# Kernel tuning notes

Measured on AMD Instinct MI355X. Metric: run time of the kernel, lower is better.

The kernel has to match this reference:

```python
import jax, jax.numpy as jnp
import numpy as np

B, T, D, H = 2, 2048, 1024, 16
Dh = D // H
MAX_LEN = 2048


def build_rope_cache(max_len, head_dim):
    theta = 10000.0 ** (-jnp.arange(0, head_dim, 2, dtype=jnp.float32) / head_dim)
    pos = jnp.arange(max_len, dtype=jnp.float32)
    angles = pos[:, None] * theta[None, :]          # [T, Dh/2]
    sin = jnp.sin(angles)[:, None, :]               # [T, 1, Dh/2]
    cos = jnp.cos(angles)[:, None, :]
    return sin, cos


def apply_rotary_pos_emb(q, k, sin, cos):
    q1, q2 = jnp.split(q, 2, axis=-1)
    k1, k2 = jnp.split(k, 2, axis=-1)
    q_out = jnp.concatenate([q1 * cos + q2 * sin, -q1 * sin + q2 * cos], axis=-1)
    k_out = jnp.concatenate([k1 * cos + k2 * sin, -k1 * sin + k2 * cos], axis=-1)
    return q_out, k_out


def setup_inputs() -> dict:
    key = jax.random.key(0)
    k1, k2, k3 = jax.random.split(key, 3)
    x = jax.random.normal(k1, (B, T, D), dtype=jnp.float32)
    W_qkv = jax.random.normal(k2, (D, 3 * D), dtype=jnp.float32) * (D ** -0.5)
    W_proj = jax.random.normal(k3, (D, D), dtype=jnp.float32) * (D ** -0.5)
    # causal mask: 1.0 where attention is disallowed (future positions)
    mask = jnp.triu(jnp.ones((T, T), dtype=jnp.float32), k=1)
    return {"x": x, "mask": mask, "W_qkv": W_qkv, "W_proj": W_proj}


def reference(x, mask, W_qkv, W_proj):
    b, t, d = x.shape
    qkv = x @ W_qkv                                  # [B,T,3D]
    q, k, v = jnp.split(qkv, 3, axis=-1)
    q = q.reshape(b, t, H, Dh)
    k = k.reshape(b, t, H, Dh)
    v = v.reshape(b, t, H, Dh)
    sin, cos = build_rope_cache(MAX_LEN, Dh)
    q, k = apply_rotary_pos_emb(q, k, sin[:t], cos[:t])
    scale = 1.0 / jnp.sqrt(jnp.float32(Dh))
    att = jnp.einsum('bthd,bThd->bhtT', q, k) * scale
    att = att + mask * -1e9                          # mask broadcasts [T,T]->[B,H,T,T]
    weights = jax.nn.softmax(att, axis=-1)
    out = jnp.einsum('bhtT,bThd->bthd', weights, v).reshape(b, t, d)
    return out @ W_proj
```

## Files before the change

### kernel.cpp

```cpp
#include <hip/hip_runtime.h>
#include <hip/hip_bf16.h>

typedef __bf16  bf16x8 __attribute__((ext_vector_type(8)));
typedef __bf16  bf16x4 __attribute__((ext_vector_type(4)));
typedef __bf16  bf16x2 __attribute__((ext_vector_type(2)));
typedef float   f32x4  __attribute__((ext_vector_type(4)));
typedef float   f32x16 __attribute__((ext_vector_type(16)));
typedef unsigned u32x4 __attribute__((ext_vector_type(4)));

#define MFMA16(a,b,c) __builtin_amdgcn_mfma_f32_16x16x32_bf16(a,b,c,0,0,0)
#define MFMA32(a,b,c) __builtin_amdgcn_mfma_f32_32x32x16_bf16(a,b,c,0,0,0)


struct bf4 { __hip_bfloat16 a,b,c,d; };

__global__ __launch_bounds__(256) void cast_f32_bf16(const float* __restrict__ in,
                                                     __hip_bfloat16* __restrict__ out,
                                                     int n4) {
  int i = blockIdx.x * 256 + threadIdx.x;
  if (i >= n4) return;
  float4 v = ((const float4*)in)[i];
  bf4 o { __float2bfloat16(v.x), __float2bfloat16(v.y),
          __float2bfloat16(v.z), __float2bfloat16(v.w) };
  ((bf4*)out)[i] = o;
}

__global__ __launch_bounds__(256) void transpose_cast(const float* __restrict__ W,
                                                      __hip_bfloat16* __restrict__ WT,
                                                      int R, int C) {
  __shared__ float tile[32][33];
  int c0 = blockIdx.x * 32, r0 = blockIdx.y * 32;
  int tx = threadIdx.x & 31, ty = threadIdx.x >> 5;
  #pragma unroll
  for (int i = 0; i < 32; i += 8)
    tile[ty + i][tx] = W[(size_t)(r0 + ty + i) * C + c0 + tx];
  __syncthreads();
  #pragma unroll
  for (int i = 0; i < 32; i += 8)
    WT[(size_t)(c0 + ty + i) * R + r0 + tx] = __float2bfloat16(tile[tx][ty + i]);
}

template <typename OutT>
__global__ __launch_bounds__(256) void gemm_bt(const __hip_bfloat16* __restrict__ A,
                                               const __hip_bfloat16* __restrict__ BT,
                                               OutT* __restrict__ C,
                                               int M, int N, int K) {
  __shared__ __hip_bfloat16 As[2][128][32];
  __shared__ __hip_bfloat16 Bs[2][128][32];
  int tid  = threadIdx.x;
  int lane = tid & 63, wid = tid >> 6;
  int wm = wid >> 1, wn = wid & 1;
  int rowBase = blockIdx.y * 128;
  int colBase = blockIdx.x * 128;
  int lr = lane & 15, lg = lane >> 4;

  f32x4 acc[4][4];
  #pragma unroll
  for (int i = 0; i < 4; ++i)
    #pragma unroll
    for (int j = 0; j < 4; ++j) acc[i][j] = f32x4{0.f,0.f,0.f,0.f};

  int nt = K >> 5;

#define GSTAGE(buf, kt)                                                                 \
  do {                                                                                  \
    int k0_ = (kt) << 5;                                                                \
    _Pragma("unroll")                                                                   \
    for (int p = 0; p < 2; ++p) {                                                       \
      int idx = p * 256 + tid;                                                          \
      int r_ = idx >> 2, sl_ = idx & 3;                                                 \
      __builtin_amdgcn_global_load_lds(                                                 \
        (const __attribute__((address_space(1))) unsigned int*)                         \
          &A[(size_t)(rowBase + r_) * K + k0_ + ((sl_ ^ (r_ & 3)) * 8)],                \
        (__attribute__((address_space(3))) unsigned int*)&As[buf][r_][sl_ * 8], 16, 0, 0);\
      __builtin_amdgcn_global_load_lds(                                                 \
        (const __attribute__((address_space(1))) unsigned int*)                         \
          &BT[(size_t)(colBase + r_) * K + k0_ + ((sl_ ^ (r_ & 3)) * 8)],               \
        (__attribute__((address_space(3))) unsigned int*)&Bs[buf][r_][sl_ * 8], 16, 0, 0);\
    }                                                                                   \
  } while (0)

  GSTAGE(0, 0);
  for (int t = 0; t < nt; ++t) {
    int cur = t & 1;
    if (t + 1 < nt) {
      GSTAGE(cur ^ 1, t + 1);
      asm volatile("s_waitcnt vmcnt(4)" ::: "memory");
    } else {
      asm volatile("s_waitcnt vmcnt(0)" ::: "memory");
    }
    __builtin_amdgcn_s_barrier();
    __builtin_amdgcn_sched_barrier(0);

    bf16x8 af[4], bfr[4];
    #pragma unroll
    for (int mf = 0; mf < 4; ++mf) {
      int row = wm*64 + mf*16 + lr;
      af[mf]  = *(const bf16x8*)&As[cur][row][((lg ^ (lr & 3)) * 8)];
    }
    #pragma unroll
    for (int nf = 0; nf < 4; ++nf) {
      int row = wn*64 + nf*16 + lr;
      bfr[nf] = *(const bf16x8*)&Bs[cur][row][((lg ^ (lr & 3)) * 8)];
    }
    #pragma unroll
    for (int mf = 0; mf < 4; ++mf)
      #pragma unroll
      for (int nf = 0; nf < 4; ++nf)
        acc[mf][nf] = MFMA16(af[mf], bfr[nf], acc[mf][nf]);

    __builtin_amdgcn_s_barrier();
  }
#undef GSTAGE

  #pragma unroll
  for (int mf = 0; mf < 4; ++mf)
    #pragma unroll
    for (int nf = 0; nf < 4; ++nf)
      #pragma unroll
      for (int r = 0; r < 4; ++r) {
        int row = rowBase + wm*64 + mf*16 + lg*4 + r;
        int col = colBase + wn*64 + nf*16 + lr;
        float v = acc[mf][nf][r];
        if constexpr (sizeof(OutT) == 2) C[(size_t)row * N + col] = __float2bfloat16(v);
        else                             C[(size_t)row * N + col] = v;
      }
}

__global__ __launch_bounds__(256) void build_sincos(float2* __restrict__ tbl) {
  int idx = blockIdx.x * 256 + threadIdx.x;
  int i = idx & 31, t = idx >> 5;
  float theta = expf(-9.210340371976184f * (float)i * 0.03125f);
  float sn, cs;
  sincosf((float)t * theta, &sn, &cs);
  tbl[idx] = float2{sn, cs};
}

__global__ __launch_bounds__(256) void rope_qk(const __hip_bfloat16* __restrict__ qkv,
                                               const float2* __restrict__ tbl,
                                               __hip_bfloat16* __restrict__ Qb,
                                               __hip_bfloat16* __restrict__ Kb) {
  int idx = blockIdx.x * 256 + threadIdx.x;
  int i = idx & 31;
  int h = (idx >> 5) & 15;
  int t = (idx >> 9) & 2047;
  int b = idx >> 20;
  size_t row = (size_t)(b * 2048 + t) * 3072;
  float q1 = __bfloat162float(qkv[row + h*64 + i]);
  float q2 = __bfloat162float(qkv[row + h*64 + 32 + i]);
  float k1 = __bfloat162float(qkv[row + 1024 + h*64 + i]);
  float k2 = __bfloat162float(qkv[row + 1024 + h*64 + 32 + i]);

  float2 sc = tbl[(t << 5) | i];
  float sn = sc.x, cs = sc.y;

  const float QS = 0.18033688011112042f;
  size_t qkbase = ((size_t)(b*16 + h) * 2048 + t) * 64;
  Qb[qkbase + i]      = __float2bfloat16(( q1*cs + q2*sn) * QS);
  Qb[qkbase + 32 + i] = __float2bfloat16((-q1*sn + q2*cs) * QS);
  Kb[qkbase + i]      = __float2bfloat16( k1*cs + k2*sn);
  Kb[qkbase + 32 + i] = __float2bfloat16(-k1*sn + k2*cs);
}

__global__ __launch_bounds__(256) void v_transpose(const __hip_bfloat16* __restrict__ qkv,
                                                   __hip_bfloat16* __restrict__ Vt) {
  __shared__ __hip_bfloat16 tile[64][66];
  int blk = blockIdx.x;
  int tb = blk & 31, hh = (blk >> 5) & 15, bb = blk >> 9;
  int t0 = tb * 64;
  int tid = threadIdx.x;
  int row = tid >> 2, dc = (tid & 3) * 16;
  const __hip_bfloat16* src = qkv + (size_t)(bb*2048 + t0 + row) * 3072 + 2048 + hh*64 + dc;
  *(bf16x8*)&tile[row][dc]     = *(const bf16x8*)&src[0];
  *(bf16x8*)&tile[row][dc + 8] = *(const bf16x8*)&src[8];
  __syncthreads();
  int d = tid >> 2, tc = (tid & 3) * 16;
  __hip_bfloat16 outv[16];
  #pragma unroll
  for (int k = 0; k < 16; ++k) outv[k] = tile[tc + k][d];
  __hip_bfloat16* dst = Vt + ((size_t)(bb*16 + hh) * 64 + d) * 2048 + t0 + tc;
  *(bf16x8*)&dst[0] = *(bf16x8*)&outv[0];
  *(bf16x8*)&dst[8] = *(bf16x8*)&outv[8];
}

__device__ __forceinline__ unsigned pk2(float lo, float hi_) {
  bf16x2 t; t[0] = (__bf16)lo; t[1] = (__bf16)hi_;
  return __builtin_bit_cast(unsigned, t);
}

__global__ __launch_bounds__(512) void attn_chunk(const __hip_bfloat16* __restrict__ Qb,
                                                  const __hip_bfloat16* __restrict__ Kb,
                                                  const __hip_bfloat16* __restrict__ Vt,
                                                  __hip_bfloat16* __restrict__ Opart,
                                                  float* __restrict__ sbuf) {
  __shared__ __hip_bfloat16 Ks[2048];
  __shared__ __hip_bfloat16 Vs[2048];
  int tid = threadIdx.x;
  int wid = tid >> 6, lane = tid & 63;
  int ql = lane & 31, hi = lane >> 5;

  int bid = blockIdx.x;
  int bh, c, jbase, lenmax; bool diag;
  if (bid < 384) {
    bh = bid / 12; int pr = bid % 12;
    if (pr < 6)       { c = 0; jbase = 16 + 8*pr; }
    else if (pr < 10) { c = 1; jbase = 32 + 8*(pr-6); }
    else              { c = 2; jbase = 48 + 8*(pr-10); }
    lenmax = 16; diag = false;
  } else {
    int e = bid - 384;
    int hh = (e < 128) ? 1 : 0;
    int e2 = e & 127;
    bh = e2 >> 2; c = e2 & 3;
    jbase = 16*c + 8*hh; lenmax = 8*hh + 8; diag = true;
  }
  int j = jbase + wid;
  int len = diag ? ((j & 15) + 1) : 16;
  int q0 = j * 32, t0 = c * 512;
  int jobid;
  if (!diag) jobid = (c == 0) ? (j - 16) : ((c == 1) ? (j + 16) : (j + 32));
  else       jobid = 96 + ((15 - (j & 15)) << 2) + c;
  int job = jobid * 32 + bh;

  const __hip_bfloat16* Qp = Qb + (size_t)bh * 2048 * 64;
  const __hip_bfloat16* Kp = Kb + (size_t)bh * 2048 * 64;
  const __hip_bfloat16* Vp = Vt + (size_t)bh * 64 * 2048;

  bf16x8 qf[4];
  #pragma unroll
  for (int cc = 0; cc < 4; ++cc)
    qf[cc] = *(const bf16x8*)&Qp[(size_t)(q0 + ql) * 64 + cc*16 + hi*8];

  f32x16 o0, o1;
  #pragma unroll
  for (int r = 0; r < 16; ++r) { o0[r] = 0.f; o1[r] = 0.f; }
  float s = 0.f;

  int kr = tid >> 3, ksl = tid & 7;
  int vjj = tid - 256, vr = vjj >> 2, vsl = vjj & 3;

  for (int it = 0; it < lenmax; ++it) {
    int kv0 = t0 + it * 32;
    if (tid < 256)
      __builtin_amdgcn_global_load_lds(
        (const __attribute__((address_space(1))) unsigned int*)&Kp[(size_t)(kv0 + kr) * 64 + ((ksl ^ (kr & 7)) * 8)],
        (__attribute__((address_space(3))) unsigned int*)&Ks[tid * 8], 16, 0, 0);
    else
      __builtin_amdgcn_global_load_lds(
        (const __attribute__((address_space(1))) unsigned int*)&Vp[(size_t)vr * 2048 + kv0 + ((vsl ^ (vr & 3)) * 8)],
        (__attribute__((address_space(3))) unsigned int*)&Vs[vjj * 8], 16, 0, 0);
    __syncthreads();

    if (it < len) {
      bf16x8 kf[4], vf[4];
      #pragma unroll
      for (int cc = 0; cc < 4; ++cc)
        kf[cc] = *(const bf16x8*)&Ks[ql * 64 + (((cc*2 + hi) ^ (ql & 7)) * 8)];
      #pragma unroll
      for (int g = 0; g < 2; ++g)
        #pragma unroll
        for (int cc = 0; cc < 2; ++cc)
          vf[g*2 + cc] = *(const bf16x8*)&Vs[(g*32 + ql) * 32 + (((cc*2 + hi) ^ (ql & 3)) * 8)];

      f32x16 st;
      #pragma unroll
      for (int r = 0; r < 16; ++r) st[r] = 0.f;
      #pragma unroll
      for (int cc = 0; cc < 4; ++cc) st = MFMA32(kf[cc], qf[cc], st);

      if (diag && it == len - 1) {
        #pragma unroll
        for (int r = 0; r < 16; ++r) {
          int kv = kv0 + (r & 3) + 8*(r >> 2) + 4*hi;
          if (kv > q0 + ql) st[r] = -1e30f;
        }
      }

      float p[16]; float ps = 0.f;
      #pragma unroll
      for (int r = 0; r < 16; ++r) { p[r] = exp2f(st[r]); ps += p[r]; }
      ps += __shfl_xor(ps, 32);
      s += ps;

      bf16x8 pb[2];
      #pragma unroll
      for (int cc = 0; cc < 2; ++cc) {
        unsigned w0 = pk2(p[cc*8+0], p[cc*8+1]);
        unsigned w1 = pk2(p[cc*8+2], p[cc*8+3]);
        unsigned w2 = pk2(p[cc*8+4], p[cc*8+5]);
        unsigned w3 = pk2(p[cc*8+6], p[cc*8+7]);
        unsigned r0 = __shfl_xor(hi ? w0 : w2, 32);
        unsigned r1 = __shfl_xor(hi ? w1 : w3, 32);
        u32x4 pw;
        pw[0] = hi ? r0 : w0;
        pw[1] = hi ? r1 : w1;
        pw[2] = hi ? w2 : r0;
        pw[3] = hi ? w3 : r1;
        pb[cc] = __builtin_bit_cast(bf16x8, pw);
      }

      o0 = MFMA32(vf[0], pb[0], o0);
      o0 = MFMA32(vf[1], pb[1], o0);
      o1 = MFMA32(vf[2], pb[0], o1);
      o1 = MFMA32(vf[3], pb[1], o1);
    }
    __syncthreads();
  }

  __hip_bfloat16* Op = Opart + (size_t)job * 2048 + ql * 64;
  #pragma unroll
  for (int rr = 0; rr < 4; ++rr) {
    bf16x4 w;
    #pragma unroll
    for (int e = 0; e < 4; ++e) w[e] = (__bf16)o0[rr*4 + e];
    *(bf16x4*)&Op[8*rr + 4*hi] = w;
  }
  #pragma unroll
  for (int rr = 0; rr < 4; ++rr) {
    bf16x4 w;
    #pragma unroll
    for (int e = 0; e < 4; ++e) w[e] = (__bf16)o1[rr*4 + e];
    *(bf16x4*)&Op[32 + 8*rr + 4*hi] = w;
  }
  if (hi == 0) sbuf[(size_t)job * 32 + ql] = s;
}

__global__ __launch_bounds__(64) void attn_combine(const __hip_bfloat16* __restrict__ Opart,
                                                   const float* __restrict__ sbuf,
                                                   __hip_bfloat16* __restrict__ Ob) {
  int bid2 = blockIdx.x;
  int j = bid2 >> 5, bh = bid2 & 31;
  int h = bh & 15, b = bh >> 4;
  int tid = threadIdx.x, ql = tid & 31, half = tid >> 5;
  int nc = (j >> 4) + 1;

  int gs[4];
  const int Sseg[3] = {0, 48, 80};
  #pragma unroll
  for (int i = 0; i < 3; ++i)
    if (i < nc - 1) gs[i] = (Sseg[i] + j - 16*(i+1)) * 32 + bh;
  gs[nc-1] = (96 + 4*(15 - (j & 15)) + (j >> 4)) * 32 + bh;

  float Ssum = 0.f;
  #pragma unroll
  for (int i = 0; i < 4; ++i)
    if (i < nc) Ssum += sbuf[(size_t)gs[i]*32 + ql];

  float acc[32];
  #pragma unroll
  for (int e = 0; e < 32; ++e) acc[e] = 0.f;
  #pragma unroll
  for (int i = 0; i < 4; ++i)
    if (i < nc) {
      const bf16x8* src = (const bf16x8*)(Opart + (size_t)gs[i]*2048 + ql*64 + half*32);
      #pragma unroll
      for (int q4 = 0; q4 < 4; ++q4) {
        bf16x8 v = src[q4];
        #pragma unroll
        for (int e = 0; e < 8; ++e) acc[q4*8 + e] += (float)v[e];
      }
    }

  float inv = 1.f / Ssum;
  size_t row = (size_t)b * 2048 + j*32 + ql;
  __hip_bfloat16* dst = Ob + row * 1024 + h*64 + half*32;
  #pragma unroll
  for (int q4 = 0; q4 < 4; ++q4) {
    bf16x8 w;
    #pragma unroll
    for (int e = 0; e < 8; ++e) w[e] = (__bf16)(acc[q4*8 + e] * inv);
    *(bf16x8*)&dst[q4*8] = w;
  }
}

extern "C" void kernel_launch(void* const* d_in, const int* in_sizes, int n_in,
                              void* d_out, int out_size, void* d_ws, size_t ws_size,
                              hipStream_t stream) {
  const float* x     = (const float*)d_in[0];
  const float* Wqkv  = (const float*)d_in[2];
  const float* Wproj = (const float*)d_in[3];
  float* out = (float*)d_out;

  char* ws = (char*)d_ws;
  const size_t MB = 1024 * 1024;
  __hip_bfloat16* xb  = (__hip_bfloat16*)(ws);
  __hip_bfloat16* Wqt = (__hip_bfloat16*)(ws +  8*MB);
  __hip_bfloat16* Wpt = (__hip_bfloat16*)(ws + 14*MB);
  __hip_bfloat16* qkv = (__hip_bfloat16*)(ws + 16*MB);
  __hip_bfloat16* Qb  = (__hip_bfloat16*)(ws + 40*MB);
  __hip_bfloat16* Kb  = (__hip_bfloat16*)(ws + 48*MB);
  __hip_bfloat16* Vt  = (__hip_bfloat16*)(ws + 56*MB);
  __hip_bfloat16* Ob  = (__hip_bfloat16*)(ws + 64*MB);
  __hip_bfloat16* Opart = (__hip_bfloat16*)(ws + 16*MB);
  float*          sbuf  = (float*)(ws + 36*MB);
  float2*         sctbl = (float2*)(ws + 8*MB);

  cast_f32_bf16<<<4096, 256, 0, stream>>>(x, xb, 1048576);
  transpose_cast<<<dim3(96, 32), 256, 0, stream>>>(Wqkv, Wqt, 1024, 3072);
  transpose_cast<<<dim3(32, 32), 256, 0, stream>>>(Wproj, Wpt, 1024, 1024);
  gemm_bt<__hip_bfloat16><<<dim3(24, 32), 256, 0, stream>>>(xb, Wqt, qkv, 4096, 3072, 1024);
  build_sincos<<<256, 256, 0, stream>>>(sctbl);
  rope_qk<<<8192, 256, 0, stream>>>(qkv, sctbl, Qb, Kb);
  v_transpose<<<1024, 256, 0, stream>>>(qkv, Vt);
  attn_chunk<<<640, 512, 0, stream>>>(Qb, Kb, Vt, Opart, sbuf);
  attn_combine<<<2048, 64, 0, stream>>>(Opart, sbuf, Ob);
  gemm_bt<float><<<dim3(8, 32), 256, 0, stream>>>(Ob, Wpt, out, 4096, 1024, 1024);
}
```

Measured before the change: 137.3 us.

## Double-buffer K/V LDS tiles in attention chunk kernel with async prefetch

Splits the K and V shared-memory tiles into two buffers and issues the global-to-LDS load for the next KV block before computing on the current one. Explicit vmcnt waits and raw barriers replace __syncthreads, so load latency can overlap with the MFMA and softmax work. This doubles LDS use per block, which may lower occupancy, and relies on hand-placed waitcnt and barriers being correct.

```diff
diff --git a/kernel.cpp b/kernel.cpp
--- a/kernel.cpp
+++ b/kernel.cpp
@@ -193,8 +193,8 @@
                                                   const __hip_bfloat16* __restrict__ Vt,
                                                   __hip_bfloat16* __restrict__ Opart,
                                                   float* __restrict__ sbuf) {
-  __shared__ __hip_bfloat16 Ks[2048];
-  __shared__ __hip_bfloat16 Vs[2048];
+  __shared__ __hip_bfloat16 Ks[2][2048];
+  __shared__ __hip_bfloat16 Vs[2][2048];
   int tid = threadIdx.x;
   int wid = tid >> 6, lane = tid & 63;
   int ql = lane & 31, hi = lane >> 5;
@@ -239,28 +239,44 @@
   int kr = tid >> 3, ksl = tid & 7;
   int vjj = tid - 256, vr = vjj >> 2, vsl = vjj & 3;
 
+#define ASTAGE(buf, it_)                                                                \
+  do {                                                                                  \
+    int kv0_ = t0 + (it_) * 32;                                                         \
+    if (tid < 256)                                                                      \
+      __builtin_amdgcn_global_load_lds(                                                 \
+        (const __attribute__((address_space(1))) unsigned int*)                         \
+          &Kp[(size_t)(kv0_ + kr) * 64 + ((ksl ^ (kr & 7)) * 8)],                       \
+        (__attribute__((address_space(3))) unsigned int*)&Ks[buf][tid * 8], 16, 0, 0);  \
+    else                                                                                \
+      __builtin_amdgcn_global_load_lds(                                                 \
+        (const __attribute__((address_space(1))) unsigned int*)                         \
+          &Vp[(size_t)vr * 2048 + kv0_ + ((vsl ^ (vr & 3)) * 8)],                       \
+        (__attribute__((address_space(3))) unsigned int*)&Vs[buf][vjj * 8], 16, 0, 0);  \
+  } while (0)
+
+  ASTAGE(0, 0);
   for (int it = 0; it < lenmax; ++it) {
-    int kv0 = t0 + it * 32;
-    if (tid < 256)
-      __builtin_amdgcn_global_load_lds(
-        (const __attribute__((address_space(1))) unsigned int*)&Kp[(size_t)(kv0 + kr) * 64 + ((ksl ^ (kr & 7)) * 8)],
-        (__attribute__((address_space(3))) unsigned int*)&Ks[tid * 8], 16, 0, 0);
-    else
-      __builtin_amdgcn_global_load_lds(
-        (const __attribute__((address_space(1))) unsigned int*)&Vp[(size_t)vr * 2048 + kv0 + ((vsl ^ (vr & 3)) * 8)],
-        (__attribute__((address_space(3))) unsigned int*)&Vs[vjj * 8], 16, 0, 0);
-    __syncthreads();
+    int cur = it & 1;
+    if (it + 1 < lenmax) {
+      ASTAGE(cur ^ 1, it + 1);
+      asm volatile("s_waitcnt vmcnt(1)" ::: "memory");
+    } else {
+      asm volatile("s_waitcnt vmcnt(0)" ::: "memory");
+    }
+    __builtin_amdgcn_s_barrier();
+    __builtin_amdgcn_sched_barrier(0);
 
     if (it < len) {
+      int kv0 = t0 + it * 32;
       bf16x8 kf[4], vf[4];
       #pragma unroll
       for (int cc = 0; cc < 4; ++cc)
-        kf[cc] = *(const bf16x8*)&Ks[ql * 64 + (((cc*2 + hi) ^ (ql & 7)) * 8)];
+        kf[cc] = *(const bf16x8*)&Ks[cur][ql * 64 + (((cc*2 + hi) ^ (ql & 7)) * 8)];
       #pragma unroll
       for (int g = 0; g < 2; ++g)
         #pragma unroll
         for (int cc = 0; cc < 2; ++cc)
-          vf[g*2 + cc] = *(const bf16x8*)&Vs[(g*32 + ql) * 32 + (((cc*2 + hi) ^ (ql & 3)) * 8)];
+          vf[g*2 + cc] = *(const bf16x8*)&Vs[cur][(g*32 + ql) * 32 + (((cc*2 + hi) ^ (ql & 3)) * 8)];
 
       f32x16 st;
       #pragma unroll
@@ -304,8 +320,9 @@
       o1 = MFMA32(vf[2], pb[0], o1);
       o1 = MFMA32(vf[3], pb[1], o1);
     }
-    __syncthreads();
-  }
+    __builtin_amdgcn_s_barrier();
+  }
+#undef ASTAGE
 
   __hip_bfloat16* Op = Opart + (size_t)job * 2048 + ql * 64;
   #pragma unroll
```

Measured after the change: 132.0 us. 1.04x faster.
